# Performance work log

Measured on AMD Instinct MI355X. Metric: run time of the kernel, lower is better.

The kernel has to match this reference:

```python
import jax, jax.numpy as jnp
from jax import lax
import numpy as np

_CUBIC = np.array([-0.01171875, -0.03515625, 0.11328125, 0.43359375,
                   0.43359375, 0.11328125, -0.03515625, -0.01171875], dtype=np.float32)


def setup_inputs() -> dict:
    key = jax.random.key(0)
    x = jax.random.normal(key, (4, 64, 128, 4096), dtype=jnp.float32)
    kernel = jnp.asarray(_CUBIC)  # fixed anti-aliasing FIR buffer (K=8)
    return {"x": x, "kernel": kernel}


def reference(x, kernel):
    # Downsample-by-2 along T with depthwise cubic FIR (diagonal weight in the
    # original => exactly a per-channel 1D convolution).
    B, C0, Fbins, T = x.shape
    K = kernel.shape[0]
    pad = K // 2 - 1  # 3 for cubic
    xr = x.reshape(-1, Fbins, T)                                  # (B*C0, F, T)
    xp = jnp.pad(xr, ((0, 0), (0, 0), (pad, pad)), mode="reflect")
    w = jnp.broadcast_to(kernel, (Fbins, 1, K))                   # depthwise OIW
    y = lax.conv_general_dilated(
        xp, w,
        window_strides=(2,),
        padding="VALID",
        dimension_numbers=("NCH", "OIH", "NCH"),
        feature_group_count=Fbins,
    )                                                             # (B*C0, F, T/2)
    return y.reshape(B, -1, Fbins, y.shape[-1])
```

## Files before the change

kernel.cpp:

```cpp
#include <hip/hip_runtime.h>


#define TLEN 4096
#define OLEN 2048
#define PAD 3
#define NTHREADS 256
#define NROWS 32768

__global__ __launch_bounds__(NTHREADS) void fir_down2_kernel(
    const float* __restrict__ x, const float* __restrict__ w,
    float* __restrict__ y)
{
    __shared__ float s[TLEN + 2 * PAD];

    const int tid = threadIdx.x;
    const long row = blockIdx.x;
    const float* __restrict__ xr = x + row * (long)TLEN;
    float* __restrict__ yr = y + row * (long)OLEN;

    const float k0 = w[0], k1 = w[1], k2 = w[2], k3 = w[3];
    const float k4 = w[4], k5 = w[5], k6 = w[6], k7 = w[7];

    const float4* __restrict__ x4 = (const float4*)xr;
#pragma unroll
    for (int j = 0; j < 4; ++j) {
        const int idx = tid + j * NTHREADS;
        const float4 v = x4[idx];
        const int p = PAD + idx * 4;
        s[p + 0] = v.x; s[p + 1] = v.y; s[p + 2] = v.z; s[p + 3] = v.w;
    }
    if (tid < PAD) {
        s[tid] = xr[PAD - tid];
        s[TLEN + PAD + tid] = xr[TLEN - 2 - tid];
    }
    __syncthreads();

#pragma unroll
    for (int it = 0; it < OLEN / NTHREADS; ++it) {
        const int t = tid + it * NTHREADS;
        const float* sp = s + 2 * t;
        const float acc = sp[0] * k0 + sp[1] * k1 + sp[2] * k2 + sp[3] * k3
                        + sp[4] * k4 + sp[5] * k5 + sp[6] * k6 + sp[7] * k7;
        yr[t] = acc;
    }
}

extern "C" void kernel_launch(void* const* d_in, const int* in_sizes, int n_in,
                              void* d_out, int out_size, void* d_ws, size_t ws_size,
                              hipStream_t stream) {
    const float* x = (const float*)d_in[0];
    const float* w = (const float*)d_in[1];
    float* y = (float*)d_out;
    fir_down2_kernel<<<NROWS, NTHREADS, 0, stream>>>(x, w, y);
}
```

Before: 144.8 us.

## Split input into even/odd polyphase LDS buffers with vectorized reads and stores

The row is deinterleaved into separate even and odd shared-memory buffers, with reflect padding folded into the buffer edges. Each thread then reads two float4s from each buffer and computes four consecutive outputs, replacing strided scalar LDS reads and scalar global stores with vector ones. Nontemporal loads and stores are added for the streaming input and output. This cuts LDS instruction count and bank conflicts but adds edge-case branches in the load loop.

```diff
diff --git a/kernel.cpp b/kernel.cpp
--- a/kernel.cpp
+++ b/kernel.cpp
@@ -3,45 +3,63 @@
 
 #define TLEN 4096
 #define OLEN 2048
-#define PAD 3
 #define NTHREADS 256
 #define NROWS 32768
 
-__global__ __launch_bounds__(NTHREADS) void fir_down2_kernel(
+typedef float f4 __attribute__((ext_vector_type(4)));
+typedef float f2 __attribute__((ext_vector_type(2)));
+
+__global__ __launch_bounds__(NTHREADS) void fir_down2_poly(
     const float* __restrict__ x, const float* __restrict__ w,
     float* __restrict__ y)
 {
-    __shared__ float s[TLEN + 2 * PAD];
+    __shared__ __align__(16) float Ebuf[2052];
+    __shared__ __align__(16) float Obuf[2052];
 
     const int tid = threadIdx.x;
     const long row = blockIdx.x;
-    const float* __restrict__ xr = x + row * (long)TLEN;
-    float* __restrict__ yr = y + row * (long)OLEN;
+    const f4* __restrict__ x4 = (const f4*)(x + row * (long)TLEN);
+    f4* __restrict__ y4 = (f4*)(y + row * (long)OLEN);
 
-    const float k0 = w[0], k1 = w[1], k2 = w[2], k3 = w[3];
-    const float k4 = w[4], k5 = w[5], k6 = w[6], k7 = w[7];
+    const float k0=w[0],k1=w[1],k2=w[2],k3=w[3],k4=w[4],k5=w[5],k6=w[6],k7=w[7];
 
-    const float4* __restrict__ x4 = (const float4*)xr;
 #pragma unroll
     for (int j = 0; j < 4; ++j) {
-        const int idx = tid + j * NTHREADS;
-        const float4 v = x4[idx];
-        const int p = PAD + idx * 4;
-        s[p + 0] = v.x; s[p + 1] = v.y; s[p + 2] = v.z; s[p + 3] = v.w;
-    }
-    if (tid < PAD) {
-        s[tid] = xr[PAD - tid];
-        s[TLEN + PAD + tid] = xr[TLEN - 2 - tid];
+        const int i = tid + j * NTHREADS;
+        const f4 v = __builtin_nontemporal_load(&x4[i]);
+        *(f2*)&Ebuf[2*i+2] = (f2){v.y, v.w};
+        *(f2*)&Obuf[2*i+2] = (f2){v.x, v.z};
+        if (i == 0) {
+            Ebuf[0] = v.w;
+            Ebuf[1] = v.y;
+            Obuf[1] = v.z;
+            Obuf[0] = 0.f;
+        }
+        if (i == 1023) {
+            Ebuf[2050] = v.y;
+            Obuf[2050] = v.z;
+            Obuf[2051] = v.x;
+            Ebuf[2051] = 0.f;
+        }
     }
     __syncthreads();
 
+    const f4* E4 = (const f4*)Ebuf;
+    const f4* O4 = (const f4*)Obuf;
 #pragma unroll
-    for (int it = 0; it < OLEN / NTHREADS; ++it) {
-        const int t = tid + it * NTHREADS;
-        const float* sp = s + 2 * t;
-        const float acc = sp[0] * k0 + sp[1] * k1 + sp[2] * k2 + sp[3] * k3
-                        + sp[4] * k4 + sp[5] * k5 + sp[6] * k6 + sp[7] * k7;
-        yr[t] = acc;
+    for (int g = 0; g < 2; ++g) {
+        const int u = tid + g * NTHREADS;
+        const f4 eA = E4[u], eB = E4[u + 1];
+        const f4 oA = O4[u], oB = O4[u + 1];
+        const float Ev[7] = {eA.x, eA.y, eA.z, eA.w, eB.x, eB.y, eB.z};
+        const float Ov[7] = {oA.y, oA.z, oA.w, oB.x, oB.y, oB.z, oB.w};
+        float o[4];
+#pragma unroll
+        for (int r = 0; r < 4; ++r)
+            o[r] = Ev[r] * k0 + Ov[r] * k1 + Ev[r+1] * k2 + Ov[r+1] * k3
+                 + Ev[r+2] * k4 + Ov[r+2] * k5 + Ev[r+3] * k6 + Ov[r+3] * k7;
+        const f4 out = {o[0], o[1], o[2], o[3]};
+        __builtin_nontemporal_store(out, &y4[u]);
     }
 }
 
@@ -51,5 +69,5 @@
     const float* x = (const float*)d_in[0];
     const float* w = (const float*)d_in[1];
     float* y = (float*)d_out;
-    fir_down2_kernel<<<NROWS, NTHREADS, 0, stream>>>(x, w, y);
+    fir_down2_poly<<<NROWS, NTHREADS, 0, stream>>>(x, w, y);
 }
```

After: 131.9 us. 1.1x faster.
